# Kernel optimization log

Measured on AMD Instinct MI355X. Metric: run time of the kernel, lower is better.

## Reference

```python
import jax, jax.numpy as jnp
import numpy as np

B, S, HID = 2, 1024, 4096
H, KV, D = 32, 8, 128
EPS = 1e-6
ROPE_THETA = 1000000.0


def _make_freqs_cis(seq_len, head_dim, theta):
    inv_freq = 1.0 / (theta ** (jnp.arange(0, head_dim, 2, dtype=jnp.float32) / head_dim))
    ang = jnp.arange(seq_len, dtype=jnp.float32)[:, None] * inv_freq[None, :]  # [S, D/2]
    emb = jnp.concatenate([ang, ang], axis=-1)                                 # [S, D]
    cos, sin = jnp.cos(emb), jnp.sin(emb)
    return jnp.stack([cos, sin, -sin], axis=0)                                 # [3, S, D]


def setup_inputs() -> dict:
    key = jax.random.key(0)
    ks = jax.random.split(key, 8)
    scale = 0.02
    return {
        "hidden_states": jax.random.normal(ks[0], (B, S, HID), dtype=jnp.float32),
        "freqs_cis": _make_freqs_cis(S, D, ROPE_THETA),
        "Wq": jax.random.normal(ks[1], (H * D, HID), dtype=jnp.float32) * scale,
        "Wk": jax.random.normal(ks[2], (KV * D, HID), dtype=jnp.float32) * scale,
        "Wv": jax.random.normal(ks[3], (KV * D, HID), dtype=jnp.float32) * scale,
        "Wo": jax.random.normal(ks[4], (HID, H * D), dtype=jnp.float32) * scale,
        "q_norm_w": jnp.ones((D,), jnp.float32) + jax.random.normal(ks[5], (D,), jnp.float32) * scale,
        "k_norm_w": jnp.ones((D,), jnp.float32) + jax.random.normal(ks[6], (D,), jnp.float32) * scale,
    }


def _rmsnorm(x, w):
    # per-head RMSNorm over last dim (rms_norm_add=False -> plain weight multiply)
    return x * jax.lax.rsqrt(jnp.mean(x * x, axis=-1, keepdims=True) + EPS) * w


def _rope(x, cos, sin, nsin):
    # matches apply_rope: e = x*cos; e[:half] += x[half:]*nsin; e[half:] += x[:half]*sin
    half = x.shape[-1] // 2
    e = x * cos
    lo = e[..., :half] + x[..., half:] * nsin[..., :half]
    hi = e[..., half:] + x[..., :half] * sin[..., half:]
    return jnp.concatenate([lo, hi], axis=-1)


def reference(hidden_states, freqs_cis, Wq, Wk, Wv, Wo, q_norm_w, k_norm_w):
    b, s, _ = hidden_states.shape
    # QKV projections (no bias)
    q = jnp.einsum("bsh,oh->bso", hidden_states, Wq).reshape(b, s, H, D).transpose(0, 2, 1, 3)
    k = jnp.einsum("bsh,oh->bso", hidden_states, Wk).reshape(b, s, KV, D).transpose(0, 2, 1, 3)
    v = jnp.einsum("bsh,oh->bso", hidden_states, Wv).reshape(b, s, KV, D).transpose(0, 2, 1, 3)
    # per-head RMSNorm (Qwen3 'gemma3' q/k norms)
    q = _rmsnorm(q, q_norm_w)
    k = _rmsnorm(k, k_norm_w)
    # RoPE
    cos, sin, nsin = freqs_cis[0], freqs_cis[1], freqs_cis[2]  # [S, D] each, broadcast over (b, heads)
    q = _rope(q, cos, sin, nsin)
    k = _rope(k, cos, sin, nsin)
    # GQA: repeat kv heads to match query heads (repeat_interleave dim=1)
    rep = H // KV
    k = jnp.repeat(k, rep, axis=1)
    v = jnp.repeat(v, rep, axis=1)
    # SDPA (no mask, past_key_value=None path)
    scale = D ** -0.5
    attn = jax.nn.softmax(jnp.einsum("bhqd,bhkd->bhqk", q, k) * scale, axis=-1)
    out = jnp.einsum("bhqk,bhkd->bhqd", attn, v)
    out = out.transpose(0, 2, 1, 3).reshape(b, s, H * D)
    return jnp.einsum("bsi,hi->bsh", out, Wo)
```

## Files before the change

### kernel.cpp

```cpp
#include <hip/hip_runtime.h>


typedef __attribute__((ext_vector_type(8))) short s8v;
typedef __attribute__((ext_vector_type(4))) float f4v;
typedef __attribute__((ext_vector_type(8))) unsigned short u8v;
typedef __attribute__((ext_vector_type(4))) float float4v;
typedef __attribute__((ext_vector_type(2))) float float2v;
typedef unsigned short us;

#define SB() __builtin_amdgcn_sched_barrier(0)

__device__ __forceinline__ void BARRIER() {
  asm volatile("" ::: "memory");
  __builtin_amdgcn_s_barrier();
  asm volatile("" ::: "memory");
}

__device__ __forceinline__ us f2b(float f) {
  unsigned u = __builtin_bit_cast(unsigned, f);
  u += 0x7fffu + ((u >> 16) & 1u);
  return (us)(u >> 16);
}
__device__ __forceinline__ float b2f(us h) {
  return __builtin_bit_cast(float, (unsigned)h << 16);
}

__device__ __forceinline__ void gload16(const void* g, void* l) {
  __builtin_amdgcn_global_load_lds(
      (const __attribute__((address_space(1))) unsigned int*)g,
      (__attribute__((address_space(3))) unsigned int*)l, 16, 0, 0);
}

__global__ __launch_bounds__(256) void cvt_all_k(const float* __restrict__ h,
                                                 const float* __restrict__ wq,
                                                 const float* __restrict__ wk,
                                                 const float* __restrict__ wv,
                                                 us* __restrict__ dst) {
  long blk = blockIdx.x;
  const float* src;
  long off;
  if (blk < 4096)        { src = h;  off = 0; }
  else if (blk < 12288)  { src = wq; off = 4096; }
  else if (blk < 14336)  { src = wk; off = 12288; }
  else                   { src = wv; off = 14336; }
  long i = (blk - off) * 2048 + (long)threadIdx.x * 8;
  long o = blk * 2048 + (long)threadIdx.x * 8;
  float4v a = *(const float4v*)(src + i);
  float4v b = *(const float4v*)(src + i + 4);
  u8v v;
  v[0] = f2b(a[0]); v[1] = f2b(a[1]); v[2] = f2b(a[2]); v[3] = f2b(a[3]);
  v[4] = f2b(b[0]); v[5] = f2b(b[1]); v[6] = f2b(b[2]); v[7] = f2b(b[3]);
  *(u8v*)(dst + o) = v;
}

template <int AH, bool F32OUT, bool CVTTAIL>
__global__ __launch_bounds__(512, 2) void gemm8p(const us* __restrict__ A,
                                                 const us* __restrict__ W,
                                                 void* __restrict__ Cv,
                                                 int K, int nkt, int ldc,
                                                 int cm, int cn, int ncn,
                                                 int nGemm,
                                                 const float* __restrict__ csrc,
                                                 us* __restrict__ cdst) {
  if constexpr (CVTTAIL) {
    if ((int)blockIdx.x >= nGemm) {
      long c = (long)((int)blockIdx.x - nGemm) * 512 + threadIdx.x;
      for (; c < 2097152; c += 64 * 512) {
        long i = c * 8;
        float4v x = *(const float4v*)(csrc + i);
        float4v y = *(const float4v*)(csrc + i + 4);
        u8v v;
        v[0] = f2b(x[0]); v[1] = f2b(x[1]); v[2] = f2b(x[2]); v[3] = f2b(x[3]);
        v[4] = f2b(y[0]); v[5] = f2b(y[1]); v[6] = f2b(y[2]); v[7] = f2b(y[3]);
        *(u8v*)(cdst + i) = v;
      }
      return;
    }
  }

  constexpr int FR = AH / 32;
  constexpr int LA = AH / 64;
  constexpr int VM = 2 * LA + 2;

  __shared__ __align__(16) us Ah[2][2][AH * 64];
  __shared__ __align__(16) us Bh[2][2][128 * 64];
  const int tid = threadIdx.x, lane = tid & 63, w = tid >> 6;
  const int wr = w >> 2, wc = w & 3;
  const int lr = lane & 15, lg = lane >> 4;

  const int xcd = (int)blockIdx.x & 7;
  const int i2 = (int)blockIdx.x >> 3;
  const int im = i2 % cm, itn = i2 / cm;
  const long m0 = (long)((xcd / ncn) * cm + im) * (2 * AH);
  const long n0 = (long)((xcd % ncn) * cn + itn) * 256;

  const int rA0 = tid >> 3;
  const int sc0 = ((tid & 7) ^ (rA0 & 7)) << 3;

#define STGH(dst, src, LOADS)                                           \
  do {                                                                  \
    const us* _s = (src);                                               \
    us* _d = (dst);                                                     \
    _Pragma("unroll") for (int l = 0; l < (LOADS); ++l)                 \
      gload16(_s + (long)(rA0 + l * 64) * K + sc0, _d + (l * 512 + tid) * 8); \
  } while (0)

  const us* Asrc = A + m0 * K;
  const us* Bsrc = W + n0 * K;
  const long hKA = (long)AH * K;
  const long hKB = (long)128 * K;

  const int ra = wr * (AH / 2) + lr, rb = wc * 32 + lr;
  const int offA0 = ra * 64 + ((lg ^ (ra & 7)) << 3);
  const int offA1 = ra * 64 + (((4 + lg) ^ (ra & 7)) << 3);
  const int offB0 = rb * 64 + ((lg ^ (rb & 7)) << 3);
  const int offB1 = rb * 64 + (((4 + lg) ^ (rb & 7)) << 3);

  f4v acc[2 * FR][4];
#pragma unroll
  for (int i = 0; i < 2 * FR; ++i)
#pragma unroll
    for (int j = 0; j < 4; ++j) acc[i][j] = (f4v){0.f, 0.f, 0.f, 0.f};

  const int nk = nkt;

  STGH(Ah[0][0], Asrc, LA);
  STGH(Bh[0][0], Bsrc, 2);
  STGH(Bh[0][1], Bsrc + hKB, 2);
  STGH(Ah[0][1], Asrc + hKA, LA);
  STGH(Ah[1][0], Asrc + 64, LA);
  STGH(Bh[1][1], Bsrc + hKB + 64, 2);
  STGH(Ah[1][1], Asrc + hKA + 64, LA);
  asm volatile("s_waitcnt vmcnt(%0)" :: "i"(VM) : "memory");
  BARRIER();

  s8v a[FR][2], b0[2][2], b1[2][2];

#define RD_A(H)                                                         \
  _Pragma("unroll") for (int f = 0; f < FR; ++f) {                      \
    a[f][0] = *(const s8v*)(&Ah[d][H][offA0 + f * 1024]);               \
    a[f][1] = *(const s8v*)(&Ah[d][H][offA1 + f * 1024]);               \
  }
#define RD_B(BB, H)                                                     \
  _Pragma("unroll") for (int g = 0; g < 2; ++g) {                       \
    BB[g][0] = *(const s8v*)(&Bh[d][H][offB0 + g * 1024]);              \
    BB[g][1] = *(const s8v*)(&Bh[d][H][offB1 + g * 1024]);              \
  }
#define QUAD(QM, QN, BB)                                                \
  __builtin_amdgcn_s_setprio(1);                                        \
  _Pragma("unroll") for (int f = 0; f < FR; ++f)                        \
  _Pragma("unroll") for (int g = 0; g < 2; ++g) {                       \
    f4v t = acc[QM * FR + f][QN * 2 + g];                               \
    t = __builtin_amdgcn_mfma_f32_16x16x32_bf16(a[f][0], BB[g][0], t, 0, 0, 0); \
    t = __builtin_amdgcn_mfma_f32_16x16x32_bf16(a[f][1], BB[g][1], t, 0, 0, 0); \
    acc[QM * FR + f][QN * 2 + g] = t;                                   \
  }                                                                     \
  __builtin_amdgcn_s_setprio(0);
#define PREMFMA()                                                       \
  BARRIER();                                                            \
  asm volatile("s_waitcnt lgkmcnt(0)" ::: "memory");                    \
  SB();

  for (int kt = 0; kt < nk; ++kt) {
    const int d = kt & 1;
    const long kb2 = (long)(kt + 2) * 64;
    const bool p1 = (kt + 1 < nk), p2 = (kt + 2 < nk);

    RD_A(0)
    RD_B(b0, 0)
    if (p1) STGH(Bh[d ^ 1][0], Bsrc + (long)(kt + 1) * 64, 2);
    PREMFMA()
    QUAD(0, 0, b0)
    BARRIER();

    RD_B(b1, 1)
    if (p2) STGH(Ah[d][0], Asrc + kb2, LA);
    PREMFMA()
    QUAD(0, 1, b1)
    BARRIER();

    RD_A(1)
    if (p2) STGH(Bh[d][1], Bsrc + hKB + kb2, 2);
    PREMFMA()
    QUAD(1, 1, b1)
    BARRIER();

    if (p2) STGH(Ah[d][1], Asrc + hKA + kb2, LA);
    PREMFMA()
    QUAD(1, 0, b0)
    if (p2) asm volatile("s_waitcnt vmcnt(%0)" :: "i"(VM) : "memory");
    else    asm volatile("s_waitcnt vmcnt(0)" ::: "memory");
    BARRIER();
  }

#pragma unroll
  for (int qm = 0; qm < 2; ++qm)
#pragma unroll
    for (int f = 0; f < FR; ++f) {
      long row = m0 + qm * AH + wr * (AH / 2) + f * 16 + lg * 4;
#pragma unroll
      for (int qn = 0; qn < 2; ++qn)
#pragma unroll
        for (int g = 0; g < 2; ++g) {
          long col = n0 + qn * 128 + wc * 32 + g * 16 + lr;
          f4v v = acc[qm * FR + f][qn * 2 + g];
          if constexpr (F32OUT) {
            float* C = (float*)Cv;
#pragma unroll
            for (int r = 0; r < 4; ++r) C[(row + r) * ldc + col] = v[r];
          } else {
            us* C = (us*)Cv;
#pragma unroll
            for (int r = 0; r < 4; ++r) C[(row + r) * ldc + col] = f2b(v[r]);
          }
        }
    }
#undef STGH
#undef RD_A
#undef RD_B
#undef QUAD
#undef PREMFMA
}

__global__ __launch_bounds__(256) void rms_rope_k(us* __restrict__ qkv,
                                                  const float* __restrict__ fc,
                                                  const float* __restrict__ kw) {
  int idx = blockIdx.x * 4 + (threadIdx.x >> 6);
  int lane = threadIdx.x & 63;
  int head = idx & 7;
  int row = idx >> 3;
  int s = row & 1023;
  us* p = qkv + (long)row * 6144 + 4096 + head * 128;
  const float* w = kw;

  unsigned v = ((const unsigned*)p)[lane];
  float x0 = b2f((us)(v & 0xffff)), x1 = b2f((us)(v >> 16));
  float ss = x0 * x0 + x1 * x1;
#pragma unroll
  for (int off = 32; off; off >>= 1) ss += __shfl_xor(ss, off);
  float r = rsqrtf(ss * (1.0f / 128.0f) + 1e-6f);
  float2v wv = ((const float2v*)w)[lane];
  float y0 = x0 * r * wv[0], y1 = x1 * r * wv[1];
  float py0 = __shfl(y0, lane ^ 32);
  float py1 = __shfl(y1, lane ^ 32);
  float2v cv = ((const float2v*)(fc + (long)s * 128))[lane];
  const float* sbase = (lane < 32) ? (fc + 2 * 1024 * 128) : (fc + 1024 * 128);
  float2v sv = ((const float2v*)(sbase + (long)s * 128))[lane];
  float e0 = y0 * cv[0] + py0 * sv[0];
  float e1 = y1 * cv[1] + py1 * sv[1];
  ((unsigned*)p)[lane] = (unsigned)f2b(e0) | ((unsigned)f2b(e1) << 16);
}

__global__ __launch_bounds__(256) void attn_k(const us* __restrict__ qkv,
                                              us* __restrict__ ao,
                                              const float* __restrict__ fc,
                                              const float* __restrict__ qw) {
  __shared__ us Kt[64 * 128];
  __shared__ us Vt[128 * 72];
  __shared__ us Pl[4 * 1024];

  const int bid = blockIdx.x;
  const int qt = bid & 15;
  const int h = (bid >> 4) & 31;
  const int b = bid >> 9;
  const int kvh = h >> 2;
  const int tid = threadIdx.x, lane = tid & 63, w = tid >> 6;
  const int lr = lane & 15, lg = lane >> 4;

  const int srow = qt * 64 + w * 16 + lr;
  const us* Qb = qkv + (long)(b * 1024 + srow) * 6144 + h * 128;
  s8v qr[4];
#pragma unroll
  for (int ks = 0; ks < 4; ++ks) qr[ks] = *(const s8v*)(Qb + ks * 32 + lg * 8);

  float ssq = 0.f;
#pragma unroll
  for (int ks = 0; ks < 4; ++ks)
#pragma unroll
    for (int j = 0; j < 8; ++j) {
      float x = b2f((us)qr[ks][j]);
      ssq += x * x;
    }
  ssq += __shfl_xor(ssq, 16);
  ssq += __shfl_xor(ssq, 32);
  const float rr = rsqrtf(ssq * (1.0f / 128.0f) + 1e-6f);

  const float* cosp = fc + (long)srow * 128;
  const float* sinp = fc + 1024 * 128 + (long)srow * 128;
  s8v qf[4];
#pragma unroll
  for (int ks = 0; ks < 4; ++ks) {
    const int d0 = ks * 32 + lg * 8;
    const int dp = d0 ^ 64;
    const float sgn = (ks < 2) ? -1.f : 1.f;
#pragma unroll
    for (int j = 0; j < 8; ++j) {
      float y  = b2f((us)qr[ks][j])     * rr * qw[d0 + j];
      float yp = b2f((us)qr[ks ^ 2][j]) * rr * qw[dp + j];
      float e = y * cosp[d0 + j] + yp * sgn * sinp[d0 + j];
      qf[ks][j] = (short)f2b(e);
    }
  }

  f4v o[8];
#pragma unroll
  for (int n = 0; n < 8; ++n) o[n] = (f4v){0.f, 0.f, 0.f, 0.f};
  float m[4], l[4];
#pragma unroll
  for (int r = 0; r < 4; ++r) { m[r] = -1e30f; l[r] = 0.f; }

  const float SL = 0.08838834764831845f * 1.4426950408889634f;
  const long krow = (long)b * 1024 * 6144 + 4096 + kvh * 128;
  const long vrow = (long)b * 1024 * 6144 + 5120 + kvh * 128;

  for (int kt = 0; kt < 16; ++kt) {
    __syncthreads();
#pragma unroll
    for (int t = 0; t < 4; ++t) {
      int c = t * 256 + tid;
      int row = c >> 4;
      int sc = (c & 15) ^ (row & 7);
      gload16(qkv + krow + (long)(kt * 64 + row) * 6144 + sc * 8, &Kt[c * 8]);
    }
#pragma unroll
    for (int t = 0; t < 2; ++t) {
      int c = t * 256 + tid;
      int kp = c & 31;
      int d0 = (c >> 5) * 8;
      const us* vsrc = qkv + vrow + (long)(kt * 64) * 6144 + d0;
      s8v va = *(const s8v*)(vsrc + (long)(2 * kp) * 6144);
      s8v vb = *(const s8v*)(vsrc + (long)(2 * kp + 1) * 6144);
#pragma unroll
      for (int i = 0; i < 8; ++i) {
        unsigned pk = (unsigned)(us)va[i] | ((unsigned)(us)vb[i] << 16);
        *(unsigned*)&Vt[(d0 + i) * 72 + 2 * kp] = pk;
      }
    }
    __syncthreads();

    f4v sacc[4];
#pragma unroll
    for (int j = 0; j < 4; ++j) sacc[j] = (f4v){0.f, 0.f, 0.f, 0.f};
    __builtin_amdgcn_s_setprio(1);
#pragma unroll
    for (int ks = 0; ks < 4; ++ks) {
#pragma unroll
      for (int j = 0; j < 4; ++j) {
        int key = j * 16 + lr;
        s8v kf = *(const s8v*)&Kt[key * 128 + (((ks * 64 + lg * 16) ^ ((key & 7) << 4)) >> 1)];
        sacc[j] = __builtin_amdgcn_mfma_f32_16x16x32_bf16(qf[ks], kf, sacc[j], 0, 0, 0);
      }
    }
    __builtin_amdgcn_s_setprio(0);

    float sm[4];
#pragma unroll
    for (int r = 0; r < 4; ++r)
      sm[r] = fmaxf(fmaxf(sacc[0][r], sacc[1][r]), fmaxf(sacc[2][r], sacc[3][r]));
#pragma unroll
    for (int off = 1; off < 16; off <<= 1)
#pragma unroll
      for (int r = 0; r < 4; ++r) sm[r] = fmaxf(sm[r], __shfl_xor(sm[r], off));
    float alpha[4];
#pragma unroll
    for (int r = 0; r < 4; ++r) {
      float nm = fmaxf(m[r], sm[r] * SL);
      alpha[r] = exp2f(m[r] - nm);
      m[r] = nm;
      l[r] *= alpha[r];
    }
#pragma unroll
    for (int n = 0; n < 8; ++n)
#pragma unroll
      for (int r = 0; r < 4; ++r) o[n][r] *= alpha[r];

    us* pw = Pl + w * 1024;
#pragma unroll
    for (int j = 0; j < 4; ++j)
#pragma unroll
      for (int r = 0; r < 4; ++r) {
        float p = exp2f(sacc[j][r] * SL - m[r]);
        l[r] += p;
        int prow = lg * 4 + r, pcol = j * 16 + lr;
        pw[(prow * 128 + ((pcol * 2) ^ ((prow & 7) << 4))) >> 1] = f2b(p);
      }

    __builtin_amdgcn_s_setprio(1);
#pragma unroll
    for (int ks = 0; ks < 2; ++ks) {
      int bo = ks * 64 + lg * 16;
      s8v pf = *(const s8v*)&Pl[w * 1024 + ((lr * 128 + (bo ^ ((lr & 7) << 4))) >> 1)];
#pragma unroll
      for (int n = 0; n < 8; ++n) {
        s8v vf = *(const s8v*)&Vt[(n * 16 + lr) * 72 + ks * 32 + lg * 8];
        o[n] = __builtin_amdgcn_mfma_f32_16x16x32_bf16(pf, vf, o[n], 0, 0, 0);
      }
    }
    __builtin_amdgcn_s_setprio(0);
  }

#pragma unroll
  for (int off = 1; off < 16; off <<= 1)
#pragma unroll
    for (int r = 0; r < 4; ++r) l[r] += __shfl_xor(l[r], off);
  float inv[4];
#pragma unroll
  for (int r = 0; r < 4; ++r) inv[r] = 1.f / l[r];
  const long ob = (long)(b * 1024 + qt * 64 + w * 16) * 4096 + h * 128;
#pragma unroll
  for (int n = 0; n < 8; ++n)
#pragma unroll
    for (int r = 0; r < 4; ++r)
      ao[ob + (long)(lg * 4 + r) * 4096 + n * 16 + lr] = f2b(o[n][r] * inv[r]);
}

extern "C" void kernel_launch(void* const* d_in, const int* in_sizes, int n_in,
                              void* d_out, int out_size, void* d_ws, size_t ws_size,
                              hipStream_t stream) {
  const float* hidden = (const float*)d_in[0];
  const float* fc     = (const float*)d_in[1];
  const float* Wq     = (const float*)d_in[2];
  const float* Wk     = (const float*)d_in[3];
  const float* Wv     = (const float*)d_in[4];
  const float* Wo     = (const float*)d_in[5];
  const float* qw     = (const float*)d_in[6];
  const float* kw     = (const float*)d_in[7];

  us* hb  = (us*)d_ws;
  us* wb  = hb + (long)2048 * 4096;
  us* wbo = wb + (long)6144 * 4096;
  us* qkv = wbo + (long)4096 * 4096;
  us* ao  = qkv + (long)2048 * 6144;

  cvt_all_k<<<16384, 256, 0, stream>>>(hidden, Wq, Wk, Wv, hb);

  gemm8p<128, false, true><<<256, 512, 0, stream>>>(
      hb, wb, qkv, 4096, 64, 6144, 4, 6, 4, 192, Wo, wbo);

  rms_rope_k<<<4096, 256, 0, stream>>>(qkv, fc, kw);

  attn_k<<<1024, 256, 0, stream>>>(qkv, ao, fc, qw);

  gemm8p<64, true, false><<<256, 512, 0, stream>>>(
      ao, wbo, d_out, 4096, 64, 4096, 8, 4, 4, 256, nullptr, nullptr);
}
```

Before: 337.5 us.

## Replace output projection GEMM with dedicated 256x128-tile double-buffered kernel

Result: faster. 322.9 us (-4.3%).

```diff
diff --git a/kernel.cpp b/kernel.cpp
--- a/kernel.cpp
+++ b/kernel.cpp
@@ -222,6 +222,111 @@
 #undef PREMFMA
 }
 
+__global__ __launch_bounds__(512) void gemm2p(const us* __restrict__ A,
+                                              const us* __restrict__ W,
+                                              float* __restrict__ C) {
+  constexpr int K = 4096, nk = 64, ldc = 4096;
+  __shared__ __align__(16) us Ab[2][256 * 64];
+  __shared__ __align__(16) us Bb[2][128 * 64];
+  const int tid = threadIdx.x, lane = tid & 63, w = tid >> 6;
+  const int wm = w & 3, wn = w >> 2;
+  const int lr = lane & 15, lg = lane >> 4;
+
+  const int xcd = (int)blockIdx.x & 7;
+  const int i2 = (int)blockIdx.x >> 3;
+  const long m0 = (long)(i2 & 7) * 256;
+  const long n0 = (long)(xcd * 4 + (i2 >> 3)) * 128;
+
+  const int rA0 = tid >> 3;
+  const int sc0 = ((tid & 7) ^ (rA0 & 7)) << 3;
+  const us* Asrc = A + m0 * K;
+  const us* Bsrc = W + n0 * K;
+
+#define STGA2(buf, src)                                                  \
+  do {                                                                   \
+    const us* _s = (src);                                                \
+    _Pragma("unroll") for (int l = 0; l < 4; ++l)                        \
+      gload16(_s + (long)(rA0 + l * 64) * K + sc0, &Ab[buf][(l * 512 + tid) * 8]); \
+  } while (0)
+#define STGB2(buf, src)                                                  \
+  do {                                                                   \
+    const us* _s = (src);                                                \
+    _Pragma("unroll") for (int l = 0; l < 2; ++l)                        \
+      gload16(_s + (long)(rA0 + l * 64) * K + sc0, &Bb[buf][(l * 512 + tid) * 8]); \
+  } while (0)
+
+  const int ra = wm * 64 + lr;
+  const int rb = wn * 64 + lr;
+  const int offA0 = ra * 64 + ((lg ^ (ra & 7)) << 3);
+  const int offA1 = ra * 64 + (((4 + lg) ^ (ra & 7)) << 3);
+  const int offB0 = rb * 64 + ((lg ^ (rb & 7)) << 3);
+  const int offB1 = rb * 64 + (((4 + lg) ^ (rb & 7)) << 3);
+
+  f4v acc[4][4];
+#pragma unroll
+  for (int f = 0; f < 4; ++f)
+#pragma unroll
+    for (int g = 0; g < 4; ++g) acc[f][g] = (f4v){0.f, 0.f, 0.f, 0.f};
+
+  STGA2(0, Asrc);
+  STGB2(0, Bsrc);
+  STGA2(1, Asrc + 64);
+  asm volatile("s_waitcnt vmcnt(4)" ::: "memory");
+  BARRIER();
+
+  for (int kt = 0; kt < nk; ++kt) {
+    const int d = kt & 1;
+    const bool p1 = (kt + 1 < nk), p2 = (kt + 2 < nk);
+
+    s8v a[4][2], b[4][2];
+#pragma unroll
+    for (int f = 0; f < 4; ++f) {
+      a[f][0] = *(const s8v*)(&Ab[d][offA0 + f * 1024]);
+      a[f][1] = *(const s8v*)(&Ab[d][offA1 + f * 1024]);
+    }
+#pragma unroll
+    for (int g = 0; g < 4; ++g) {
+      b[g][0] = *(const s8v*)(&Bb[d][offB0 + g * 1024]);
+      b[g][1] = *(const s8v*)(&Bb[d][offB1 + g * 1024]);
+    }
+    if (p1) STGB2(d ^ 1, Bsrc + (long)(kt + 1) * 64);
+    asm volatile("s_waitcnt lgkmcnt(0)" ::: "memory");
+    BARRIER();
+    if (p2) STGA2(d, Asrc + (long)(kt + 2) * 64);
+
+    __builtin_amdgcn_s_setprio(1);
+#pragma unroll
+    for (int f = 0; f < 4; ++f)
+#pragma unroll
+      for (int g = 0; g < 4; ++g) {
+        f4v t = acc[f][g];
+        t = __builtin_amdgcn_mfma_f32_16x16x32_bf16(a[f][0], b[g][0], t, 0, 0, 0);
+        t = __builtin_amdgcn_mfma_f32_16x16x32_bf16(a[f][1], b[g][1], t, 0, 0, 0);
+        acc[f][g] = t;
+      }
+    __builtin_amdgcn_s_setprio(0);
+
+    if (p2)      asm volatile("s_waitcnt vmcnt(4)" ::: "memory");
+    else if (p1) asm volatile("s_waitcnt vmcnt(0)" ::: "memory");
+    else         asm volatile("s_waitcnt vmcnt(0)" ::: "memory");
+    BARRIER();
+  }
+
+#pragma unroll
+  for (int f = 0; f < 4; ++f) {
+    long row = m0 + wm * 64 + f * 16 + lg * 4;
+#pragma unroll
+    for (int g = 0; g < 4; ++g) {
+      long col = n0 + wn * 64 + g * 16 + lr;
+      f4v v = acc[f][g];
+#pragma unroll
+      for (int r = 0; r < 4; ++r) C[(row + r) * ldc + col] = v[r];
+    }
+  }
+#undef STGA2
+#undef STGB2
+}
+
 __global__ __launch_bounds__(256) void rms_rope_k(us* __restrict__ qkv,
                                                   const float* __restrict__ fc,
                                                   const float* __restrict__ kw) {
@@ -231,7 +336,6 @@
   int row = idx >> 3;
   int s = row & 1023;
   us* p = qkv + (long)row * 6144 + 4096 + head * 128;
-  const float* w = kw;
 
   unsigned v = ((const unsigned*)p)[lane];
   float x0 = b2f((us)(v & 0xffff)), x1 = b2f((us)(v >> 16));
@@ -239,7 +343,7 @@
 #pragma unroll
   for (int off = 32; off; off >>= 1) ss += __shfl_xor(ss, off);
   float r = rsqrtf(ss * (1.0f / 128.0f) + 1e-6f);
-  float2v wv = ((const float2v*)w)[lane];
+  float2v wv = ((const float2v*)kw)[lane];
   float y0 = x0 * r * wv[0], y1 = x1 * r * wv[1];
   float py0 = __shfl(y0, lane ^ 32);
   float py1 = __shfl(y1, lane ^ 32);
@@ -441,6 +545,5 @@
 
   attn_k<<<1024, 256, 0, stream>>>(qkv, ao, fc, qw);
 
-  gemm8p<64, true, false><<<256, 512, 0, stream>>>(
-      ao, wbo, d_out, 4096, 64, 4096, 8, 4, 4, 256, nullptr, nullptr);
-}
+  gemm2p<<<256, 512, 0, stream>>>(ao, wbo, (float*)d_out);
+}
```

## Split-K output projection, 128-row attention blocks, and lazy softmax rescaling

Applied to the files above, without the earlier changes.

New measurement: 309.7 us. 8.2% less time.

```diff
diff --git a/kernel.cpp b/kernel.cpp
--- a/kernel.cpp
+++ b/kernel.cpp
@@ -53,7 +53,21 @@
   *(u8v*)(dst + o) = v;
 }
 
-template <int AH, bool F32OUT, bool CVTTAIL>
+__global__ __launch_bounds__(256) void add2_k(const float* __restrict__ p,
+                                              float* __restrict__ out, long n) {
+  long i = ((long)blockIdx.x * 256 + threadIdx.x) * 8;
+  float4v a0 = *(const float4v*)(p + i);
+  float4v b0 = *(const float4v*)(p + i + 4);
+  float4v a1 = *(const float4v*)(p + n + i);
+  float4v b1 = *(const float4v*)(p + n + i + 4);
+  float4v ra, rb;
+#pragma unroll
+  for (int k = 0; k < 4; ++k) { ra[k] = a0[k] + a1[k]; rb[k] = b0[k] + b1[k]; }
+  *(float4v*)(out + i) = ra;
+  *(float4v*)(out + i + 4) = rb;
+}
+
+template <int AH, bool F32OUT, bool CVTTAIL, bool SPLITK>
 __global__ __launch_bounds__(512, 2) void gemm8p(const us* __restrict__ A,
                                                  const us* __restrict__ W,
                                                  void* __restrict__ Cv,
@@ -90,9 +104,20 @@
 
   const int xcd = (int)blockIdx.x & 7;
   const int i2 = (int)blockIdx.x >> 3;
-  const int im = i2 % cm, itn = i2 / cm;
-  const long m0 = (long)((xcd / ncn) * cm + im) * (2 * AH);
-  const long n0 = (long)((xcd % ncn) * cn + itn) * 256;
+  long m0, n0, koff = 0;
+  float* Cf = (float*)Cv;
+  if constexpr (SPLITK) {
+    const int ks = i2 >> 4;
+    const int r = i2 & 15;
+    m0 = (long)((xcd >> 2) * 4 + (r & 3)) * 256;
+    n0 = (long)((xcd & 3) * 4 + (r >> 2)) * 256;
+    koff = (long)ks * nkt * 64;
+    Cf += (long)ks * 2048 * 4096;
+  } else {
+    const int im = i2 % cm, itn = i2 / cm;
+    m0 = (long)((xcd / ncn) * cm + im) * (2 * AH);
+    n0 = (long)((xcd % ncn) * cn + itn) * 256;
+  }
 
   const int rA0 = tid >> 3;
   const int sc0 = ((tid & 7) ^ (rA0 & 7)) << 3;
@@ -105,8 +130,8 @@
       gload16(_s + (long)(rA0 + l * 64) * K + sc0, _d + (l * 512 + tid) * 8); \
   } while (0)
 
-  const us* Asrc = A + m0 * K;
-  const us* Bsrc = W + n0 * K;
+  const us* Asrc = A + m0 * K + koff;
+  const us* Bsrc = W + n0 * K + koff;
   const long hKA = (long)AH * K;
   const long hKB = (long)128 * K;
 
@@ -205,9 +230,8 @@
           long col = n0 + qn * 128 + wc * 32 + g * 16 + lr;
           f4v v = acc[qm * FR + f][qn * 2 + g];
           if constexpr (F32OUT) {
-            float* C = (float*)Cv;
-#pragma unroll
-            for (int r = 0; r < 4; ++r) C[(row + r) * ldc + col] = v[r];
+#pragma unroll
+            for (int r = 0; r < 4; ++r) Cf[(row + r) * ldc + col] = v[r];
           } else {
             us* C = (us*)Cv;
 #pragma unroll
@@ -231,7 +255,6 @@
   int row = idx >> 3;
   int s = row & 1023;
   us* p = qkv + (long)row * 6144 + 4096 + head * 128;
-  const float* w = kw;
 
   unsigned v = ((const unsigned*)p)[lane];
   float x0 = b2f((us)(v & 0xffff)), x1 = b2f((us)(v >> 16));
@@ -239,7 +262,7 @@
 #pragma unroll
   for (int off = 32; off; off >>= 1) ss += __shfl_xor(ss, off);
   float r = rsqrtf(ss * (1.0f / 128.0f) + 1e-6f);
-  float2v wv = ((const float2v*)w)[lane];
+  float2v wv = ((const float2v*)kw)[lane];
   float y0 = x0 * r * wv[0], y1 = x1 * r * wv[1];
   float py0 = __shfl(y0, lane ^ 32);
   float py1 = __shfl(y1, lane ^ 32);
@@ -251,23 +274,23 @@
   ((unsigned*)p)[lane] = (unsigned)f2b(e0) | ((unsigned)f2b(e1) << 16);
 }
 
-__global__ __launch_bounds__(256) void attn_k(const us* __restrict__ qkv,
+__global__ __launch_bounds__(512) void attn_k(const us* __restrict__ qkv,
                                               us* __restrict__ ao,
                                               const float* __restrict__ fc,
                                               const float* __restrict__ qw) {
   __shared__ us Kt[64 * 128];
   __shared__ us Vt[128 * 72];
-  __shared__ us Pl[4 * 1024];
+  __shared__ us Pl[8 * 1024];
 
   const int bid = blockIdx.x;
-  const int qt = bid & 15;
-  const int h = (bid >> 4) & 31;
-  const int b = bid >> 9;
+  const int qt = bid & 7;
+  const int h = (bid >> 3) & 31;
+  const int b = bid >> 8;
   const int kvh = h >> 2;
   const int tid = threadIdx.x, lane = tid & 63, w = tid >> 6;
   const int lr = lane & 15, lg = lane >> 4;
 
-  const int srow = qt * 64 + w * 16 + lr;
+  const int srow = qt * 128 + w * 16 + lr;
   const us* Qb = qkv + (long)(b * 1024 + srow) * 6144 + h * 128;
   s8v qr[4];
 #pragma unroll
@@ -316,15 +339,14 @@
   for (int kt = 0; kt < 16; ++kt) {
     __syncthreads();
 #pragma unroll
-    for (int t = 0; t < 4; ++t) {
-      int c = t * 256 + tid;
+    for (int t = 0; t < 2; ++t) {
+      int c = t * 512 + tid;
       int row = c >> 4;
       int sc = (c & 15) ^ (row & 7);
       gload16(qkv + krow + (long)(kt * 64 + row) * 6144 + sc * 8, &Kt[c * 8]);
     }
-#pragma unroll
-    for (int t = 0; t < 2; ++t) {
-      int c = t * 256 + tid;
+    {
+      int c = tid;
       int kp = c & 31;
       int d0 = (c >> 5) * 8;
       const us* vsrc = qkv + vrow + (long)(kt * 64) * 6144 + d0;
@@ -361,18 +383,20 @@
     for (int off = 1; off < 16; off <<= 1)
 #pragma unroll
       for (int r = 0; r < 4; ++r) sm[r] = fmaxf(sm[r], __shfl_xor(sm[r], off));
-    float alpha[4];
-#pragma unroll
-    for (int r = 0; r < 4; ++r) {
-      float nm = fmaxf(m[r], sm[r] * SL);
-      alpha[r] = exp2f(m[r] - nm);
-      m[r] = nm;
-      l[r] *= alpha[r];
-    }
-#pragma unroll
-    for (int n = 0; n < 8; ++n)
-#pragma unroll
-      for (int r = 0; r < 4; ++r) o[n][r] *= alpha[r];
+    bool ok = true;
+#pragma unroll
+    for (int r = 0; r < 4; ++r) ok = ok && (sm[r] * SL <= m[r] + 8.f);
+    if (!__all(ok)) {
+#pragma unroll
+      for (int r = 0; r < 4; ++r) {
+        float nm = fmaxf(m[r], sm[r] * SL);
+        float alpha = exp2f(m[r] - nm);
+        m[r] = nm;
+        l[r] *= alpha;
+#pragma unroll
+        for (int n = 0; n < 8; ++n) o[n][r] *= alpha;
+      }
+    }
 
     us* pw = Pl + w * 1024;
 #pragma unroll
@@ -406,7 +430,7 @@
   float inv[4];
 #pragma unroll
   for (int r = 0; r < 4; ++r) inv[r] = 1.f / l[r];
-  const long ob = (long)(b * 1024 + qt * 64 + w * 16) * 4096 + h * 128;
+  const long ob = (long)(b * 1024 + qt * 128 + w * 16) * 4096 + h * 128;
 #pragma unroll
   for (int n = 0; n < 8; ++n)
 #pragma unroll
@@ -431,16 +455,19 @@
   us* wbo = wb + (long)6144 * 4096;
   us* qkv = wbo + (long)4096 * 4096;
   us* ao  = qkv + (long)2048 * 6144;
+  float* part = (float*)d_ws;
 
   cvt_all_k<<<16384, 256, 0, stream>>>(hidden, Wq, Wk, Wv, hb);
 
-  gemm8p<128, false, true><<<256, 512, 0, stream>>>(
+  gemm8p<128, false, true, false><<<256, 512, 0, stream>>>(
       hb, wb, qkv, 4096, 64, 6144, 4, 6, 4, 192, Wo, wbo);
 
   rms_rope_k<<<4096, 256, 0, stream>>>(qkv, fc, kw);
 
-  attn_k<<<1024, 256, 0, stream>>>(qkv, ao, fc, qw);
-
-  gemm8p<64, true, false><<<256, 512, 0, stream>>>(
-      ao, wbo, d_out, 4096, 64, 4096, 8, 4, 4, 256, nullptr, nullptr);
-}
+  attn_k<<<512, 512, 0, stream>>>(qkv, ao, fc, qw);
+
+  gemm8p<128, true, false, true><<<256, 512, 0, stream>>>(
+      ao, wbo, part, 4096, 32, 4096, 0, 0, 0, 256, nullptr, nullptr);
+
+  add2_k<<<4096, 256, 0, stream>>>(part, (float*)d_out, (long)2048 * 4096);
+}
```
